# Optimization experiments

Measured on AMD Instinct MI355X. Metric: run time of the kernel, lower is better.

The kernel has to match this reference:

```python
import jax, jax.numpy as jnp
import numpy as np

ALPHA = 0.2       # LeakyReLU negative slope
NEG_INF = -9e15   # matches torch's -9000000000000000.0 masking constant


def setup_inputs() -> dict:
    key = jax.random.key(0)
    k1, k2, k3, k4 = jax.random.split(key, 4)
    N, Cin, T, V = 16, 64, 512, 64   # in_channels == out_channels == V == C (forced by module math)
    x = jax.random.normal(k1, (N, Cin, T, V), dtype=jnp.float32)
    # K=3 adjacency partitions with 0/1 entries; forward sums over dim 0 and masks where sum > 0
    A = jax.random.randint(k2, (3, V, V), 0, 2).astype(jnp.float32)
    # learned params (xavier-ish scale)
    W = jax.random.normal(k3, (V, V), dtype=jnp.float32) * 0.15
    a = jax.random.normal(k4, (2 * Cin, 1), dtype=jnp.float32) * 0.15
    return {"x": x, "A": A, "W": W, "a": a}


def reference(x, A, W, a):
    # x: [N, C, T, V_in]; W contracts the vertex dim (last axis), as in torch.matmul(x, W)
    x = jnp.einsum('nctv,vu->nctu', x, W)
    N, C, T, V = x.shape
    xf = x.transpose(0, 2, 3, 1).reshape(N * T, V, C)   # [B, V, C], B = N*T
    Asum = jnp.sum(A, axis=0)                           # [V, V]
    # e[b,i,j] = leakyrelu(cat(x_i, x_j) @ a) = leakyrelu(x_i@a1 + x_j@a2)
    a1, a2 = a[:C, 0], a[C:, 0]                         # [C], [C]
    f = xf @ a1                                         # [B, V]
    g = xf @ a2                                         # [B, V]
    e = jax.nn.leaky_relu(f[:, :, None] + g[:, None, :], ALPHA)  # [B, V, V]
    att = jnp.where(Asum[None, :, :] > 0, e, NEG_INF)
    att = jax.nn.softmax(att, axis=2)
    # dropout is identity in eval mode
    out = jnp.einsum('bij,bjc->bic', att, xf)           # [B, V, C]
    return out.reshape(N, T, V, C).transpose(0, 3, 1, 2)  # [N, C, T, V]
```

## Files before the change

### kernel.cpp

```cpp
#include <hip/hip_runtime.h>
#include <hip/hip_bf16.h>


using bf16x8 = __attribute__((ext_vector_type(8))) short;
using f32x4  = __attribute__((ext_vector_type(4))) float;
typedef unsigned long long ull;

constexpr float ALPHA = 0.2f;

__device__ __forceinline__ unsigned short f2bf(float f) {
    union { __hip_bfloat16 h; unsigned short s; } u;
    u.h = __float2bfloat16(f);
    return u.s;
}

__global__ void prep_kernel(const float* __restrict__ A,
                            const float* __restrict__ W,
                            unsigned short* __restrict__ Wt,
                            ull* __restrict__ maskT,
                            ull* __restrict__ rowzero) {
    __shared__ unsigned short part[64][4];
    __shared__ ull rowm[64];
    const int tid = threadIdx.x;
    {
        const int v = tid & 63, q = tid >> 6;
        #pragma unroll 4
        for (int m = 0; m < 16; ++m) {
            const int u = 16 * q + m;
            Wt[v * 64 + u] = f2bf(W[u * 64 + v]);
        }
    }
    {
        const int i = tid >> 2, q = tid & 3;
        const float4* a0 = (const float4*)(A + i * 64 + q * 16);
        const float4* a1 = (const float4*)(A + 4096 + i * 64 + q * 16);
        const float4* a2 = (const float4*)(A + 8192 + i * 64 + q * 16);
        unsigned m16 = 0;
        #pragma unroll
        for (int j4 = 0; j4 < 4; ++j4) {
            float4 s0 = a0[j4], s1 = a1[j4], s2 = a2[j4];
            if (s0.x + s1.x + s2.x > 0.f) m16 |= 1u << (4 * j4 + 0);
            if (s0.y + s1.y + s2.y > 0.f) m16 |= 1u << (4 * j4 + 1);
            if (s0.z + s1.z + s2.z > 0.f) m16 |= 1u << (4 * j4 + 2);
            if (s0.w + s1.w + s2.w > 0.f) m16 |= 1u << (4 * j4 + 3);
        }
        part[i][q] = (unsigned short)m16;
    }
    __syncthreads();
    if (tid < 64) {
        ull m = (ull)part[tid][0] | ((ull)part[tid][1] << 16)
              | ((ull)part[tid][2] << 32) | ((ull)part[tid][3] << 48);
        rowm[tid] = m;
        ull bz = __ballot(m == 0ull);
        if (tid == 0) rowzero[0] = bz;
    }
    __syncthreads();
    if (tid < 64) {
        ull mt = 0;
        for (int i = 0; i < 64; ++i) mt |= ((rowm[i] >> tid) & 1ull) << i;
        maskT[tid] = mt;
    }
}

__global__ __launch_bounds__(256, 6) void gat_kernel(
    const float* __restrict__ x,
    const float* __restrict__ a,
    const unsigned short* __restrict__ Wt,
    const ull* __restrict__ maskT,
    const ull* __restrict__ rowzero_p,
    float* __restrict__ out)
{
    __shared__ unsigned short XbYb[64 * 72];
    __shared__ unsigned short WtPb[64 * 72];
    __shared__ float fpart[4][64];
    __shared__ float gpart[4][64];

    const int tid  = threadIdx.x;
    const int b    = blockIdx.x;
    const int n    = b >> 9, t = b & 511;
    const int w    = tid >> 6, lane = tid & 63;
    const int fr   = lane & 15;
    const int hi   = lane >> 4;
    const int fk   = hi * 8;

    const ull mT = maskT[lane];
    const ull rz = rowzero_p[0];
    const float4 a1v = *(const float4*)&a[16 * w + 4 * hi];
    const float4 a2v = *(const float4*)&a[64 + 16 * w + 4 * hi];

    {
        const int c = tid >> 2, q = tid & 3;
        const float* xp = x + (size_t)n * 2097152 + (size_t)c * 32768 + (size_t)t * 64 + q * 16;
        float4 v0 = ((const float4*)xp)[0];
        float4 v1 = ((const float4*)xp)[1];
        float4 v2 = ((const float4*)xp)[2];
        float4 v3 = ((const float4*)xp)[3];
        union { bf16x8 v; unsigned short s[8]; } u0, u1;
        u0.s[0]=f2bf(v0.x); u0.s[1]=f2bf(v0.y); u0.s[2]=f2bf(v0.z); u0.s[3]=f2bf(v0.w);
        u0.s[4]=f2bf(v1.x); u0.s[5]=f2bf(v1.y); u0.s[6]=f2bf(v1.z); u0.s[7]=f2bf(v1.w);
        u1.s[0]=f2bf(v2.x); u1.s[1]=f2bf(v2.y); u1.s[2]=f2bf(v2.z); u1.s[3]=f2bf(v2.w);
        u1.s[4]=f2bf(v3.x); u1.s[5]=f2bf(v3.y); u1.s[6]=f2bf(v3.z); u1.s[7]=f2bf(v3.w);
        *(bf16x8*)&XbYb[c * 72 + q * 16]     = u0.v;
        *(bf16x8*)&XbYb[c * 72 + q * 16 + 8] = u1.v;
    }
    #pragma unroll
    for (int p = 0; p < 2; ++p) {
        const int r  = (tid >> 3) + 32 * p;
        const int cc = (tid & 7) * 8;
        *(bf16x8*)&WtPb[r * 72 + cc] = *(const bf16x8*)&Wt[r * 64 + cc];
    }
    __syncthreads();

    {
        f32x4 acc[4] = {{0,0,0,0},{0,0,0,0},{0,0,0,0},{0,0,0,0}};
        #pragma unroll
        for (int kc = 0; kc < 2; ++kc) {
            bf16x8 af = *(const bf16x8*)&XbYb[(16 * w + fr) * 72 + 32 * kc + fk];
            #pragma unroll
            for (int cb = 0; cb < 4; ++cb) {
                bf16x8 bfr = *(const bf16x8*)&WtPb[(16 * cb + fr) * 72 + 32 * kc + fk];
                acc[cb] = __builtin_amdgcn_mfma_f32_16x16x32_bf16(af, bfr, acc[cb], 0, 0, 0);
            }
        }
        #pragma unroll
        for (int cb = 0; cb < 4; ++cb) {
            #pragma unroll
            for (int r = 0; r < 4; ++r)
                XbYb[(16 * w + 4 * hi + r) * 72 + 16 * cb + fr] = f2bf(acc[cb][r]);
            float F = acc[cb][0]*a1v.x + acc[cb][1]*a1v.y + acc[cb][2]*a1v.z + acc[cb][3]*a1v.w;
            float G = acc[cb][0]*a2v.x + acc[cb][1]*a2v.y + acc[cb][2]*a2v.z + acc[cb][3]*a2v.w;
            F += __shfl_xor(F, 16, 64); F += __shfl_xor(F, 32, 64);
            G += __shfl_xor(G, 16, 64); G += __shfl_xor(G, 32, 64);
            if (lane < 16) {
                fpart[w][16 * cb + lane] = F;
                gpart[w][16 * cb + lane] = G;
            }
        }
    }
    __syncthreads();

    {
        const float gj = (gpart[0][lane] + gpart[1][lane]) + (gpart[2][lane] + gpart[3][lane]);
        const int myv = 16 * w + fr;
        const float ftot = (fpart[0][myv] + fpart[1][myv]) + (fpart[2][myv] + fpart[3][myv]);
        #pragma unroll
        for (int k = 0; k < 16; ++k) {
            const int i = 16 * w + k;
            const float fi = __int_as_float(
                __builtin_amdgcn_readlane(__float_as_int(ftot), k));
            const float s0 = fi + gj;
            const float e  = fmaxf(s0, ALPHA * s0);
            const bool keep = (mT >> i) & 1ull;
            const bool zrow = (rz >> i) & 1ull;
            const float p = zrow ? 1.0f : (keep ? __expf(e) : 0.0f);
            WtPb[i * 72 + lane] = f2bf(p);
        }
    }
    __syncthreads();

    {
        f32x4 acc2[4] = {{0,0,0,0},{0,0,0,0},{0,0,0,0},{0,0,0,0}};
        f32x4 accS[4] = {{0,0,0,0},{0,0,0,0},{0,0,0,0},{0,0,0,0}};
        union { bf16x8 v; unsigned short s[8]; } ones;
        #pragma unroll
        for (int j = 0; j < 8; ++j) ones.s[j] = 0x3f80;
        #pragma unroll
        for (int kc = 0; kc < 2; ++kc) {
            bf16x8 af = *(const bf16x8*)&XbYb[(16 * w + fr) * 72 + 32 * kc + fk];
            #pragma unroll
            for (int cb = 0; cb < 4; ++cb) {
                bf16x8 bfr = *(const bf16x8*)&WtPb[(16 * cb + fr) * 72 + 32 * kc + fk];
                acc2[cb] = __builtin_amdgcn_mfma_f32_16x16x32_bf16(af, bfr, acc2[cb], 0, 0, 0);
                accS[cb] = __builtin_amdgcn_mfma_f32_16x16x32_bf16(ones.v, bfr, accS[cb], 0, 0, 0);
            }
        }
        float* op = out + (size_t)n * 2097152 + (size_t)t * 64;
        #pragma unroll
        for (int cb = 0; cb < 4; ++cb) {
            const float rs  = __builtin_amdgcn_rcpf(accS[cb][0]);
            const int   col = 16 * cb + fr;
            #pragma unroll
            for (int r = 0; r < 4; ++r) {
                const int row = 16 * w + 4 * hi + r;
                op[(size_t)row * 32768 + col] = acc2[cb][r] * rs;
            }
        }
    }
}

extern "C" void kernel_launch(void* const* d_in, const int* in_sizes, int n_in,
                              void* d_out, int out_size, void* d_ws, size_t ws_size,
                              hipStream_t stream) {
    const float* x = (const float*)d_in[0];
    const float* A = (const float*)d_in[1];
    const float* W = (const float*)d_in[2];
    const float* a = (const float*)d_in[3];
    float* out = (float*)d_out;
    unsigned short* Wt = (unsigned short*)d_ws;
    ull* maskT   = (ull*)((char*)d_ws + 8192);
    ull* rowzero = (ull*)((char*)d_ws + 8704);

    prep_kernel<<<1, 256, 0, stream>>>(A, W, Wt, maskT, rowzero);
    gat_kernel<<<16 * 512, 256, 0, stream>>>(x, a, Wt, maskT, rowzero, out);
}
```

Measured before the change: 53.10 us.

## Swap MFMA operand roles for output GEMM to vectorize stores and shrink row-sum MFMAs

Recasts the final attention-times-features product so each wave's own probability rows become the A operand and the feature matrix the B operand. The row-sum normalizer then needs only two MFMAs per wave instead of eight, and each lane's four accumulator values lie along the vertex dimension. That layout allows one float4 store per output row instead of scalar strided stores. It cuts MFMA count and global store instructions, at the cost of a different LDS read pattern for the feature operand.

```diff
diff --git a/kernel.cpp b/kernel.cpp
--- a/kernel.cpp
+++ b/kernel.cpp
@@ -159,31 +159,32 @@
     __syncthreads();
 
     {
+        union { bf16x8 v; unsigned short s[8]; } ones;
+        #pragma unroll
+        for (int j = 0; j < 8; ++j) ones.s[j] = 0x3f80;
+        bf16x8 pb0 = *(const bf16x8*)&WtPb[(16 * w + fr) * 72 + fk];
+        bf16x8 pb1 = *(const bf16x8*)&WtPb[(16 * w + fr) * 72 + 32 + fk];
+        f32x4 accS = {0, 0, 0, 0};
+        accS = __builtin_amdgcn_mfma_f32_16x16x32_bf16(pb0, ones.v, accS, 0, 0, 0);
+        accS = __builtin_amdgcn_mfma_f32_16x16x32_bf16(pb1, ones.v, accS, 0, 0, 0);
         f32x4 acc2[4] = {{0,0,0,0},{0,0,0,0},{0,0,0,0},{0,0,0,0}};
-        f32x4 accS[4] = {{0,0,0,0},{0,0,0,0},{0,0,0,0},{0,0,0,0}};
-        union { bf16x8 v; unsigned short s[8]; } ones;
-        #pragma unroll
-        for (int j = 0; j < 8; ++j) ones.s[j] = 0x3f80;
-        #pragma unroll
-        for (int kc = 0; kc < 2; ++kc) {
-            bf16x8 af = *(const bf16x8*)&XbYb[(16 * w + fr) * 72 + 32 * kc + fk];
-            #pragma unroll
-            for (int cb = 0; cb < 4; ++cb) {
-                bf16x8 bfr = *(const bf16x8*)&WtPb[(16 * cb + fr) * 72 + 32 * kc + fk];
-                acc2[cb] = __builtin_amdgcn_mfma_f32_16x16x32_bf16(af, bfr, acc2[cb], 0, 0, 0);
-                accS[cb] = __builtin_amdgcn_mfma_f32_16x16x32_bf16(ones.v, bfr, accS[cb], 0, 0, 0);
-            }
-        }
-        float* op = out + (size_t)n * 2097152 + (size_t)t * 64;
-        #pragma unroll
-        for (int cb = 0; cb < 4; ++cb) {
-            const float rs  = __builtin_amdgcn_rcpf(accS[cb][0]);
-            const int   col = 16 * cb + fr;
-            #pragma unroll
-            for (int r = 0; r < 4; ++r) {
-                const int row = 16 * w + 4 * hi + r;
-                op[(size_t)row * 32768 + col] = acc2[cb][r] * rs;
-            }
+        #pragma unroll
+        for (int rb = 0; rb < 4; ++rb) {
+            bf16x8 y0 = *(const bf16x8*)&XbYb[(16 * rb + fr) * 72 + fk];
+            bf16x8 y1 = *(const bf16x8*)&XbYb[(16 * rb + fr) * 72 + 32 + fk];
+            acc2[rb] = __builtin_amdgcn_mfma_f32_16x16x32_bf16(pb0, y0, acc2[rb], 0, 0, 0);
+            acc2[rb] = __builtin_amdgcn_mfma_f32_16x16x32_bf16(pb1, y1, acc2[rb], 0, 0, 0);
+        }
+        float rs0 = __builtin_amdgcn_rcpf(accS[0]);
+        float rs1 = __builtin_amdgcn_rcpf(accS[1]);
+        float rs2 = __builtin_amdgcn_rcpf(accS[2]);
+        float rs3 = __builtin_amdgcn_rcpf(accS[3]);
+        float* op = out + (size_t)n * 2097152 + (size_t)t * 64 + 16 * w + 4 * hi;
+        #pragma unroll
+        for (int rb = 0; rb < 4; ++rb) {
+            float4 o = make_float4(acc2[rb][0] * rs0, acc2[rb][1] * rs1,
+                                   acc2[rb][2] * rs2, acc2[rb][3] * rs3);
+            *(float4*)&op[(size_t)(16 * rb + fr) * 32768] = o;
         }
     }
 }
```

New measurement: 54.40 us. 2.5% more time.

## Process two timesteps per block with upfront loads; split prep across two blocks

Applied to the files above, without the earlier changes.

Each GAT block now handles two consecutive timesteps. Both timesteps' x rows are loaded and converted to bf16 in registers at the start, so the second global load overlaps the first timestep's compute, and the grid is halved. The prep kernel splits the W transpose and mask construction into two independent blocks. The cost is more registers per thread and an extra barrier between iterations, which could lower occupancy under the existing launch bounds.

```diff
diff --git a/kernel.cpp b/kernel.cpp
--- a/kernel.cpp
+++ b/kernel.cpp
@@ -19,17 +19,18 @@
                             unsigned short* __restrict__ Wt,
                             ull* __restrict__ maskT,
                             ull* __restrict__ rowzero) {
-    __shared__ unsigned short part[64][4];
-    __shared__ ull rowm[64];
     const int tid = threadIdx.x;
-    {
+    if (blockIdx.x == 1) {
         const int v = tid & 63, q = tid >> 6;
         #pragma unroll 4
         for (int m = 0; m < 16; ++m) {
             const int u = 16 * q + m;
             Wt[v * 64 + u] = f2bf(W[u * 64 + v]);
         }
-    }
+        return;
+    }
+    __shared__ unsigned short part[64][4];
+    __shared__ ull rowm[64];
     {
         const int i = tid >> 2, q = tid & 3;
         const float4* a0 = (const float4*)(A + i * 64 + q * 16);
@@ -76,8 +77,9 @@
     __shared__ float gpart[4][64];
 
     const int tid  = threadIdx.x;
-    const int b    = blockIdx.x;
-    const int n    = b >> 9, t = b & 511;
+    const int bb   = blockIdx.x;
+    const int n    = bb >> 8;
+    const int t0   = (bb & 255) << 1;
     const int w    = tid >> 6, lane = tid & 63;
     const int fr   = lane & 15;
     const int hi   = lane >> 4;
@@ -88,101 +90,121 @@
     const float4 a1v = *(const float4*)&a[16 * w + 4 * hi];
     const float4 a2v = *(const float4*)&a[64 + 16 * w + 4 * hi];
 
+    const int c = tid >> 2, q = tid & 3;
+    const float* xp = x + (size_t)n * 2097152 + (size_t)c * 32768
+                        + (size_t)t0 * 64 + q * 16;
+    bf16x8 x0a, x0b, x1a, x1b;
     {
-        const int c = tid >> 2, q = tid & 3;
-        const float* xp = x + (size_t)n * 2097152 + (size_t)c * 32768 + (size_t)t * 64 + q * 16;
         float4 v0 = ((const float4*)xp)[0];
         float4 v1 = ((const float4*)xp)[1];
         float4 v2 = ((const float4*)xp)[2];
         float4 v3 = ((const float4*)xp)[3];
-        union { bf16x8 v; unsigned short s[8]; } u0, u1;
-        u0.s[0]=f2bf(v0.x); u0.s[1]=f2bf(v0.y); u0.s[2]=f2bf(v0.z); u0.s[3]=f2bf(v0.w);
-        u0.s[4]=f2bf(v1.x); u0.s[5]=f2bf(v1.y); u0.s[6]=f2bf(v1.z); u0.s[7]=f2bf(v1.w);
-        u1.s[0]=f2bf(v2.x); u1.s[1]=f2bf(v2.y); u1.s[2]=f2bf(v2.z); u1.s[3]=f2bf(v2.w);
-        u1.s[4]=f2bf(v3.x); u1.s[5]=f2bf(v3.y); u1.s[6]=f2bf(v3.z); u1.s[7]=f2bf(v3.w);
-        *(bf16x8*)&XbYb[c * 72 + q * 16]     = u0.v;
-        *(bf16x8*)&XbYb[c * 72 + q * 16 + 8] = u1.v;
-    }
+        float4 w0 = ((const float4*)(xp + 64))[0];
+        float4 w1 = ((const float4*)(xp + 64))[1];
+        float4 w2 = ((const float4*)(xp + 64))[2];
+        float4 w3 = ((const float4*)(xp + 64))[3];
+        union { bf16x8 v; unsigned short s[8]; } u;
+        u.s[0]=f2bf(v0.x); u.s[1]=f2bf(v0.y); u.s[2]=f2bf(v0.z); u.s[3]=f2bf(v0.w);
+        u.s[4]=f2bf(v1.x); u.s[5]=f2bf(v1.y); u.s[6]=f2bf(v1.z); u.s[7]=f2bf(v1.w);
+        x0a = u.v;
+        u.s[0]=f2bf(v2.x); u.s[1]=f2bf(v2.y); u.s[2]=f2bf(v2.z); u.s[3]=f2bf(v2.w);
+        u.s[4]=f2bf(v3.x); u.s[5]=f2bf(v3.y); u.s[6]=f2bf(v3.z); u.s[7]=f2bf(v3.w);
+        x0b = u.v;
+        u.s[0]=f2bf(w0.x); u.s[1]=f2bf(w0.y); u.s[2]=f2bf(w0.z); u.s[3]=f2bf(w0.w);
+        u.s[4]=f2bf(w1.x); u.s[5]=f2bf(w1.y); u.s[6]=f2bf(w1.z); u.s[7]=f2bf(w1.w);
+        x1a = u.v;
+        u.s[0]=f2bf(w2.x); u.s[1]=f2bf(w2.y); u.s[2]=f2bf(w2.z); u.s[3]=f2bf(w2.w);
+        u.s[4]=f2bf(w3.x); u.s[5]=f2bf(w3.y); u.s[6]=f2bf(w3.z); u.s[7]=f2bf(w3.w);
+        x1b = u.v;
+    }
+
     #pragma unroll
-    for (int p = 0; p < 2; ++p) {
-        const int r  = (tid >> 3) + 32 * p;
-        const int cc = (tid & 7) * 8;
-        *(bf16x8*)&WtPb[r * 72 + cc] = *(const bf16x8*)&Wt[r * 64 + cc];
-    }
-    __syncthreads();
-
-    {
-        f32x4 acc[4] = {{0,0,0,0},{0,0,0,0},{0,0,0,0},{0,0,0,0}};
+    for (int tt = 0; tt < 2; ++tt) {
+        if (tt) __syncthreads();
+
+        *(bf16x8*)&XbYb[c * 72 + q * 16]     = tt ? x1a : x0a;
+        *(bf16x8*)&XbYb[c * 72 + q * 16 + 8] = tt ? x1b : x0b;
         #pragma unroll
-        for (int kc = 0; kc < 2; ++kc) {
-            bf16x8 af = *(const bf16x8*)&XbYb[(16 * w + fr) * 72 + 32 * kc + fk];
+        for (int p = 0; p < 2; ++p) {
+            const int r  = (tid >> 3) + 32 * p;
+            const int cc = (tid & 7) * 8;
+            *(bf16x8*)&WtPb[r * 72 + cc] = *(const bf16x8*)&Wt[r * 64 + cc];
+        }
+        __syncthreads();
+
+        {
+            f32x4 acc[4] = {{0,0,0,0},{0,0,0,0},{0,0,0,0},{0,0,0,0}};
+            #pragma unroll
+            for (int kc = 0; kc < 2; ++kc) {
+                bf16x8 af = *(const bf16x8*)&XbYb[(16 * w + fr) * 72 + 32 * kc + fk];
+                #pragma unroll
+                for (int cb = 0; cb < 4; ++cb) {
+                    bf16x8 bfr = *(const bf16x8*)&WtPb[(16 * cb + fr) * 72 + 32 * kc + fk];
+                    acc[cb] = __builtin_amdgcn_mfma_f32_16x16x32_bf16(af, bfr, acc[cb], 0, 0, 0);
+                }
+            }
             #pragma unroll
             for (int cb = 0; cb < 4; ++cb) {
-                bf16x8 bfr = *(const bf16x8*)&WtPb[(16 * cb + fr) * 72 + 32 * kc + fk];
-                acc[cb] = __builtin_amdgcn_mfma_f32_16x16x32_bf16(af, bfr, acc[cb], 0, 0, 0);
-            }
-        }
-        #pragma unroll
-        for (int cb = 0; cb < 4; ++cb) {
-            #pragma unroll
-            for (int r = 0; r < 4; ++r)
-                XbYb[(16 * w + 4 * hi + r) * 72 + 16 * cb + fr] = f2bf(acc[cb][r]);
-            float F = acc[cb][0]*a1v.x + acc[cb][1]*a1v.y + acc[cb][2]*a1v.z + acc[cb][3]*a1v.w;
-            float G = acc[cb][0]*a2v.x + acc[cb][1]*a2v.y + acc[cb][2]*a2v.z + acc[cb][3]*a2v.w;
-            F += __shfl_xor(F, 16, 64); F += __shfl_xor(F, 32, 64);
-            G += __shfl_xor(G, 16, 64); G += __shfl_xor(G, 32, 64);
-            if (lane < 16) {
-                fpart[w][16 * cb + lane] = F;
-                gpart[w][16 * cb + lane] = G;
-            }
-        }
-    }
-    __syncthreads();
-
-    {
-        const float gj = (gpart[0][lane] + gpart[1][lane]) + (gpart[2][lane] + gpart[3][lane]);
-        const int myv = 16 * w + fr;
-        const float ftot = (fpart[0][myv] + fpart[1][myv]) + (fpart[2][myv] + fpart[3][myv]);
-        #pragma unroll
-        for (int k = 0; k < 16; ++k) {
-            const int i = 16 * w + k;
-            const float fi = __int_as_float(
-                __builtin_amdgcn_readlane(__float_as_int(ftot), k));
-            const float s0 = fi + gj;
-            const float e  = fmaxf(s0, ALPHA * s0);
-            const bool keep = (mT >> i) & 1ull;
-            const bool zrow = (rz >> i) & 1ull;
-            const float p = zrow ? 1.0f : (keep ? __expf(e) : 0.0f);
-            WtPb[i * 72 + lane] = f2bf(p);
-        }
-    }
-    __syncthreads();
-
-    {
-        f32x4 acc2[4] = {{0,0,0,0},{0,0,0,0},{0,0,0,0},{0,0,0,0}};
-        f32x4 accS[4] = {{0,0,0,0},{0,0,0,0},{0,0,0,0},{0,0,0,0}};
-        union { bf16x8 v; unsigned short s[8]; } ones;
-        #pragma unroll
-        for (int j = 0; j < 8; ++j) ones.s[j] = 0x3f80;
-        #pragma unroll
-        for (int kc = 0; kc < 2; ++kc) {
-            bf16x8 af = *(const bf16x8*)&XbYb[(16 * w + fr) * 72 + 32 * kc + fk];
+                #pragma unroll
+                for (int r = 0; r < 4; ++r)
+                    XbYb[(16 * w + 4 * hi + r) * 72 + 16 * cb + fr] = f2bf(acc[cb][r]);
+                float F = acc[cb][0]*a1v.x + acc[cb][1]*a1v.y + acc[cb][2]*a1v.z + acc[cb][3]*a1v.w;
+                float G = acc[cb][0]*a2v.x + acc[cb][1]*a2v.y + acc[cb][2]*a2v.z + acc[cb][3]*a2v.w;
+                F += __shfl_xor(F, 16, 64); F += __shfl_xor(F, 32, 64);
+                G += __shfl_xor(G, 16, 64); G += __shfl_xor(G, 32, 64);
+                if (lane < 16) {
+                    fpart[w][16 * cb + lane] = F;
+                    gpart[w][16 * cb + lane] = G;
+                }
+            }
+        }
+        __syncthreads();
+
+        {
+            const float gj = (gpart[0][lane] + gpart[1][lane]) + (gpart[2][lane] + gpart[3][lane]);
+            const int myv = 16 * w + fr;
+            const float ftot = (fpart[0][myv] + fpart[1][myv]) + (fpart[2][myv] + fpart[3][myv]);
+            #pragma unroll
+            for (int k = 0; k < 16; ++k) {
+                const int i = 16 * w + k;
+                const float fi = __int_as_float(
+                    __builtin_amdgcn_readlane(__float_as_int(ftot), k));
+                const float s0 = fi + gj;
+                const float e  = fmaxf(s0, ALPHA * s0);
+                const bool keep = (mT >> i) & 1ull;
+                const bool zrow = (rz >> i) & 1ull;
+                const float p = zrow ? 1.0f : (keep ? __expf(e) : 0.0f);
+                WtPb[i * 72 + lane] = f2bf(p);
+            }
+        }
+        __syncthreads();
+
+        {
+            f32x4 acc2[4] = {{0,0,0,0},{0,0,0,0},{0,0,0,0},{0,0,0,0}};
+            f32x4 accS[4] = {{0,0,0,0},{0,0,0,0},{0,0,0,0},{0,0,0,0}};
+            union { bf16x8 v; unsigned short s[8]; } ones;
+            #pragma unroll
+            for (int j = 0; j < 8; ++j) ones.s[j] = 0x3f80;
+            #pragma unroll
+            for (int kc = 0; kc < 2; ++kc) {
+                bf16x8 af = *(const bf16x8*)&XbYb[(16 * w + fr) * 72 + 32 * kc + fk];
+                #pragma unroll
+                for (int cb = 0; cb < 4; ++cb) {
+                    bf16x8 bfr = *(const bf16x8*)&WtPb[(16 * cb + fr) * 72 + 32 * kc + fk];
+                    acc2[cb] = __builtin_amdgcn_mfma_f32_16x16x32_bf16(af, bfr, acc2[cb], 0, 0, 0);
+                    accS[cb] = __builtin_amdgcn_mfma_f32_16x16x32_bf16(ones.v, bfr, accS[cb], 0, 0, 0);
+                }
+            }
+            float* op = out + (size_t)n * 2097152 + (size_t)(t0 + tt) * 64;
             #pragma unroll
             for (int cb = 0; cb < 4; ++cb) {
-                bf16x8 bfr = *(const bf16x8*)&WtPb[(16 * cb + fr) * 72 + 32 * kc + fk];
-                acc2[cb] = __builtin_amdgcn_mfma_f32_16x16x32_bf16(af, bfr, acc2[cb], 0, 0, 0);
-                accS[cb] = __builtin_amdgcn_mfma_f32_16x16x32_bf16(ones.v, bfr, accS[cb], 0, 0, 0);
-            }
-        }
-        float* op = out + (size_t)n * 2097152 + (size_t)t * 64;
-        #pragma unroll
-        for (int cb = 0; cb < 4; ++cb) {
-            const float rs  = __builtin_amdgcn_rcpf(accS[cb][0]);
-            const int   col = 16 * cb + fr;
-            #pragma unroll
-            for (int r = 0; r < 4; ++r) {
-                const int row = 16 * w + 4 * hi + r;
-                op[(size_t)row * 32768 + col] = acc2[cb][r] * rs;
+                const float rs  = __builtin_amdgcn_rcpf(accS[cb][0]);
+                const int   col = 16 * cb + fr;
+                #pragma unroll
+                for (int r = 0; r < 4; ++r) {
+                    const int row = 16 * w + 4 * hi + r;
+                    op[(size_t)row * 32768 + col] = acc2[cb][r] * rs;
+                }
             }
         }
     }
@@ -200,6 +222,6 @@
     ull* maskT   = (ull*)((char*)d_ws + 8192);
     ull* rowzero = (ull*)((char*)d_ws + 8704);
 
-    prep_kernel<<<1, 256, 0, stream>>>(A, W, Wt, maskT, rowzero);
-    gat_kernel<<<16 * 512, 256, 0, stream>>>(x, a, Wt, maskT, rowzero, out);
-}
+    prep_kernel<<<2, 256, 0, stream>>>(A, W, Wt, maskT, rowzero);
+    gat_kernel<<<4096, 256, 0, stream>>>(x, a, Wt, maskT, rowzero, out);
+}
```

New measurement: 134.6 us. 2.53x slower.
